# Optimization experiments

Hardware: AMD Instinct MI355X
Metric: run time of the kernel (lower is better)

The kernel has to match this reference:

```python
import jax, jax.numpy as jnp
import numpy as np
from jax import lax

B, H, W = 1, 128, 128
KS = 3
N = KS * KS  # 9 deformable sampling points
BN_EPS = 1e-5


def conv2d(x, w, padding=0, stride=1):
    return lax.conv_general_dilated(x, w, (stride, stride),
                                    [(padding, padding), (padding, padding)],
                                    dimension_numbers=('NCHW', 'OIHW', 'NCHW'))


def bn_eval(x, gamma, beta, mean, var):
    scale = gamma / jnp.sqrt(var + BN_EPS)
    return x * scale[None, :, None, None] + (beta - mean * scale)[None, :, None, None]


def upsample_bilinear_ac(x, oh, ow):
    # F.interpolate(mode='bilinear', align_corners=True), separable gather
    b, c, h, w = x.shape
    ys = jnp.linspace(0.0, h - 1.0, oh)
    xs = jnp.linspace(0.0, w - 1.0, ow)
    y0 = jnp.floor(ys).astype(jnp.int32)
    y1 = jnp.minimum(y0 + 1, h - 1)
    wy = (ys - y0).astype(x.dtype)[None, None, :, None]
    x0 = jnp.floor(xs).astype(jnp.int32)
    x1 = jnp.minimum(x0 + 1, w - 1)
    wx = (xs - x0).astype(x.dtype)
    r = x[:, :, y0, :] * (1.0 - wy) + x[:, :, y1, :] * wy
    return r[:, :, :, x0] * (1.0 - wx) + r[:, :, :, x1] * wx


def deform_conv(x, p_w, p_b, dc_w, pad=1):
    # DeformConv2d(inc, outc, ks=3, padding=1, modulation=False):
    # offsets from a 3x3 conv, bilinear gather at p0 + p_n + offset on the
    # zero-padded input, then 3x3 kernel contraction over the 9 samples.
    b, c, h, w = x.shape
    off = conv2d(x, p_w, padding=1) + p_b[None, :, None, None]  # (b, 2N, h, w)
    rng = jnp.arange(KS, dtype=x.dtype) - (KS - 1) // 2          # [-1, 0, 1]
    pnx, pny = jnp.meshgrid(rng, rng, indexing='ij')
    # absolute sampling coords in padded frame, (b, h, w, N)
    px = jnp.transpose(off[:, :N], (0, 2, 3, 1)) + pnx.ravel() + jnp.arange(1, h + 1, dtype=x.dtype)[None, :, None, None]
    py = jnp.transpose(off[:, N:], (0, 2, 3, 1)) + pny.ravel() + jnp.arange(1, w + 1, dtype=x.dtype)[None, None, :, None]
    Hp, Wp = h + 2 * pad, w + 2 * pad
    xp = jnp.pad(x, ((0, 0), (0, 0), (pad, pad), (pad, pad))).reshape(b, c, Hp * Wp)
    fx = jnp.floor(px)
    fy = jnp.floor(py)
    x0f = jnp.clip(fx, 0, Hp - 1)
    x1f = jnp.clip(fx + 1.0, 0, Hp - 1)
    y0f = jnp.clip(fy, 0, Wp - 1)
    y1f = jnp.clip(fy + 1.0, 0, Wp - 1)
    pxc = jnp.clip(px, 0, Hp - 1)
    pyc = jnp.clip(py, 0, Wp - 1)

    def gather(qxf, qyf):
        idx = (qxf.astype(jnp.int32) * Wp + qyf.astype(jnp.int32)).reshape(b, 1, h * w * N)
        g = jnp.take_along_axis(xp, jnp.broadcast_to(idx, (b, c, h * w * N)), axis=2)
        return g.reshape(b, c, h, w, N)

    g_lt = (1.0 + (x0f - pxc)) * (1.0 + (y0f - pyc))
    g_rb = (1.0 - (x1f - pxc)) * (1.0 - (y1f - pyc))
    g_lb = (1.0 + (x0f - pxc)) * (1.0 - (y1f - pyc))
    g_rt = (1.0 - (x1f - pxc)) * (1.0 + (y0f - pyc))
    x_off = (g_lt[:, None] * gather(x0f, y0f) + g_rb[:, None] * gather(x1f, y1f)
             + g_lb[:, None] * gather(x0f, y1f) + g_rt[:, None] * gather(x1f, y0f))
    # conv(kernel=3, stride=3) on the rearranged samples == contraction over N
    return jnp.einsum('bchwk,ock->bohw', x_off, dc_w.reshape(dc_w.shape[0], c, N))


def _forward(x, low_level_feat, fm_w, fs_w, p_w, p_b, dc_w,
             lc1_w, bn1_gamma, bn1_beta, bn1_mean, bn1_var,
             lc2_w, bn2_gamma, bn2_beta, bn2_mean, bn2_var):
    xu = upsample_bilinear_ac(x, H, W)                       # (B,256,128,128)
    Z = low_level_feat                                       # AdaptiveAvgPool2d((128,128)) is identity on 128x128 input
    v = jax.nn.sigmoid(jnp.einsum('oc,bchw->bohw', fm_w, Z))
    u = jnp.einsum('bchk,bckw->bchw', low_level_feat, v) + low_level_feat
    Cf = jnp.einsum('oc,bchw->bohw', fs_w, u)
    cc = jnp.concatenate([xu, Cf], axis=1)                   # (B,512,128,128)
    fam = deform_conv(cc, p_w, p_b, dc_w) + Cf
    up1 = jax.nn.relu(bn_eval(conv2d(fam, lc1_w, padding=1), bn1_gamma, bn1_beta, bn1_mean, bn1_var))
    up2 = jax.nn.relu(bn_eval(conv2d(up1, lc2_w, padding=1), bn2_gamma, bn2_beta, bn2_mean, bn2_var))
    return up1, up2


def setup_inputs():
    key = jax.random.key(0)
    ks = jax.random.split(key, 12)
    f32 = jnp.float32
    return {
        'x': jax.random.normal(ks[0], (B, 256, 32, 32), f32),
        'low_level_feat': jax.random.normal(ks[1], (B, 256, H, W), f32),
        'fm_w': jax.random.normal(ks[2], (256, 256), f32) * 0.0625,
        'fs_w': jax.random.normal(ks[3], (256, 256), f32) * 0.0625,
        'p_w': jax.random.normal(ks[4], (2 * N, 512, 3, 3), f32) * 0.01,
        'p_b': jnp.zeros((2 * N,), f32),
        'dc_w': jax.random.normal(ks[5], (256, 512, 3, 3), f32) * 0.02,
        'lc1_w': jax.random.normal(ks[6], (256, 256, 3, 3), f32) * 0.02,
        'bn1_gamma': jnp.ones((256,), f32),
        'bn1_beta': jnp.zeros((256,), f32),
        'bn1_mean': jax.random.normal(ks[7], (256,), f32) * 0.1,
        'bn1_var': jax.random.uniform(ks[8], (256,), f32) + 0.5,
        'lc2_w': jax.random.normal(ks[9], (256, 256, 3, 3), f32) * 0.02,
        'bn2_gamma': jnp.ones((256,), f32),
        'bn2_beta': jnp.zeros((256,), f32),
        'bn2_mean': jax.random.normal(ks[10], (256,), f32) * 0.1,
        'bn2_var': jax.random.uniform(ks[11], (256,), f32) + 0.5,
    }


def reference(x, low_level_feat, fm_w, fs_w, p_w, p_b, dc_w,
              lc1_w, bn1_gamma, bn1_beta, bn1_mean, bn1_var,
              lc2_w, bn2_gamma, bn2_beta, bn2_mean, bn2_var):
    return _forward(x, low_level_feat, fm_w, fs_w, p_w, p_b, dc_w,
                    lc1_w, bn1_gamma, bn1_beta, bn1_mean, bn1_var,
                    lc2_w, bn2_gamma, bn2_beta, bn2_mean, bn2_var)
```

## Files before the change

### kernel.cpp

```cpp
#include <hip/hip_runtime.h>
#include <math.h>

#define HW   16384
#define PS   16900

typedef __attribute__((ext_vector_type(8))) short bf16x8;
typedef __attribute__((ext_vector_type(4))) float f32x4;

__device__ inline unsigned short f2bf(float x) {
    unsigned int u = __float_as_uint(x);
    unsigned int r = (u + 0x7fffu + ((u >> 16) & 1u)) >> 16;
    return (unsigned short)r;
}
__device__ inline float bf2f(unsigned short h) {
    return __uint_as_float(((unsigned int)h) << 16);
}

__global__ __launch_bounds__(256) void zero_ringP2_k(unsigned short* __restrict__ b0,
                                                     unsigned short* __restrict__ b1) {
    int t = blockIdx.x * 256 + threadIdx.x;
    if (t >= 2 * 520 * 32) return;
    unsigned short* base = (t >= 520 * 32) ? b1 : b0;
    int tt = (t >= 520 * 32) ? t - 520 * 32 : t;
    int ck = (tt & 31) << 3, rp = tt >> 5;
    int row, col;
    if (rp < 130)      { row = 0;   col = rp; }
    else if (rp < 260) { row = 129; col = rp - 130; }
    else {
        int rem = rp - 260;
        if (rem >= 256) return;
        row = 1 + (rem >> 1); col = (rem & 1) ? 129 : 0;
    }
    bf16x8 z = (bf16x8){0, 0, 0, 0, 0, 0, 0, 0};
    *(bf16x8*)(base + (size_t)(row * 130 + col) * 256 + ck) = z;
}

__global__ __launch_bounds__(256) void ringT_k(unsigned short* __restrict__ ccT) {
    int t = blockIdx.x * 256 + threadIdx.x;
    if (t >= 520 * 256) return;
    int ci = t & 255, rp = t >> 8;
    int row, col;
    if (rp < 130)      { row = 0;   col = rp; }
    else if (rp < 260) { row = 129; col = rp - 130; }
    else {
        int rem = rp - 260;
        if (rem >= 256) return;
        row = 1 + (rem >> 1); col = (rem & 1) ? 129 : 0;
    }
    ccT[(size_t)(row * 130 + col) * 512 + 256 + ci] = 0;
}

__global__ __launch_bounds__(256) void xT_k(const float* __restrict__ x,
                                            float* __restrict__ xT) {
    int t = blockIdx.x * 256 + threadIdx.x;
    int c = t & 255, pos = t >> 8;
    xT[t] = x[(size_t)c * 1024 + pos];
}

__global__ __launch_bounds__(256) void up_cvtT_k(const float* __restrict__ xT,
                                                 unsigned short* __restrict__ ccT) {
    int pix = blockIdx.x;
    int c = threadIdx.x;
    int r = pix / 130, s = pix - r * 130;
    float val = 0.0f;
    if (r >= 1 && r <= 128 && s >= 1 && s <= 128) {
        int i = r - 1, j = s - 1;
        float yf = (float)i * (31.0f / 127.0f);
        float xf = (float)j * (31.0f / 127.0f);
        int y0 = min((int)yf, 31); int y1 = min(y0 + 1, 31);
        int x0 = min((int)xf, 31); int x1 = min(x0 + 1, 31);
        float wy = yf - (float)y0, wx = xf - (float)x0;
        float v00 = xT[(size_t)(y0 * 32 + x0) * 256 + c];
        float v01 = xT[(size_t)(y0 * 32 + x1) * 256 + c];
        float v10 = xT[(size_t)(y1 * 32 + x0) * 256 + c];
        float v11 = xT[(size_t)(y1 * 32 + x1) * 256 + c];
        float a = v00 * (1.0f - wx) + v01 * wx;
        float b = v10 * (1.0f - wx) + v11 * wx;
        val = a * (1.0f - wy) + b * wy;
    }
    ccT[(size_t)pix * 512 + c] = f2bf(val);
}

__global__ __launch_bounds__(256) void cvtT_tile_k(const float* __restrict__ src,
                                                   unsigned short* __restrict__ dst) {
    __shared__ float Ls[64][65];
    int px0 = blockIdx.x << 6;
    int c0  = blockIdx.y << 6;
    int t = threadIdx.x;
    int pxl = t & 63, cq = t >> 6;
#pragma unroll
    for (int it = 0; it < 16; ++it) {
        int cl = (it << 2) + cq;
        Ls[cl][pxl] = src[(size_t)(c0 + cl) * HW + px0 + pxl];
    }
    __syncthreads();
    int c8 = (t & 7) << 3;
    int pxb = t >> 3;
#pragma unroll
    for (int rr = 0; rr < 2; ++rr) {
        int px = pxb + (rr << 5);
        unsigned short pk[8];
#pragma unroll
        for (int e = 0; e < 8; ++e) pk[e] = f2bf(Ls[c8 + e][px]);
        *(bf16x8*)(dst + (size_t)(px0 + px) * 256 + c0 + c8) = *(bf16x8*)pk;
    }
}

__global__ __launch_bounds__(256) void w2bf_k(const float* __restrict__ a,
                                              const float* __restrict__ b,
                                              unsigned short* __restrict__ da,
                                              unsigned short* __restrict__ db) {
    int t = blockIdx.x * 256 + threadIdx.x;
    if (t >= 65536) return;
    da[t] = f2bf(a[t]);
    db[t] = f2bf(b[t]);
}

__global__ __launch_bounds__(256) void u_matmul_k(const float* __restrict__ llf,
                                                  const float* __restrict__ v,
                                                  float* __restrict__ u) {
    int c = blockIdx.y;
    const float* L = llf + (size_t)c * HW;
    const float* V = v   + (size_t)c * HW;
    float*       U = u   + (size_t)c * HW;
    int tid = threadIdx.x;
    int ty = tid >> 4, tx = tid & 15;
    int r0 = (blockIdx.x << 6) + (ty << 2);
    int w0 = tx << 3;
    float acc[4][8] = {};
    for (int k = 0; k < 128; ++k) {
        float a[4];
#pragma unroll
        for (int i = 0; i < 4; ++i) a[i] = L[(r0 + i) * 128 + k];
        float4 b0 = *(const float4*)(V + k * 128 + w0);
        float4 b1 = *(const float4*)(V + k * 128 + w0 + 4);
        float bv[8] = {b0.x, b0.y, b0.z, b0.w, b1.x, b1.y, b1.z, b1.w};
#pragma unroll
        for (int i = 0; i < 4; ++i)
#pragma unroll
            for (int j = 0; j < 8; ++j) acc[i][j] += a[i] * bv[j];
    }
#pragma unroll
    for (int i = 0; i < 4; ++i) {
#pragma unroll
        for (int j = 0; j < 8; ++j) acc[i][j] += L[(r0 + i) * 128 + w0 + j];
        *(float4*)(U + (r0 + i) * 128 + w0)     = make_float4(acc[i][0], acc[i][1], acc[i][2], acc[i][3]);
        *(float4*)(U + (r0 + i) * 128 + w0 + 4) = make_float4(acc[i][4], acc[i][5], acc[i][6], acc[i][7]);
    }
}

__global__ __launch_bounds__(256) void tr_dcwF9_k(const float* __restrict__ w,
                                                  unsigned short* __restrict__ dst) {
    int t = blockIdx.x * 256 + threadIdx.x;
    if (t >= 1179648) return;
    int e    = t & 7;
    int lane = (t >> 3) & 63;
    int f    = t >> 9;
    int mi   = f & 1;
    int s    = (f >> 1) & 1;
    int wv   = (f >> 2) & 7;
    int ch   = f >> 5;
    int kt   = ch >> 3;
    int o = (wv << 5) + (mi << 4) + (lane & 15);
    int c = ((ch & 7) << 6) + (s << 5) + ((lane >> 4) << 3) + e;
    dst[t] = f2bf(w[(size_t)o * 4608 + c * 9 + kt]);
}

__global__ __launch_bounds__(256) void tr_lcF2_k(const float* __restrict__ w1,
                                                 const float* __restrict__ w2,
                                                 unsigned short* __restrict__ d1,
                                                 unsigned short* __restrict__ d2) {
    const float* w = blockIdx.y ? w2 : w1;
    unsigned short* dst = blockIdx.y ? d2 : d1;
    int t = blockIdx.x * 256 + threadIdx.x;
    if (t >= 589824) return;
    int e    = t & 7;
    int lane = (t >> 3) & 63;
    int mi   = (t >> 9) & 3;
    int kss  = (t >> 11) & 7;
    int wo   = (t >> 14) & 3;
    int kt   = t >> 16;
    int o = (wo << 6) + (mi << 4) + (lane & 15);
    int c = (kss << 5) + ((lane >> 4) << 3) + e;
    dst[t] = f2bf(w[(size_t)o * 2304 + c * 9 + kt]);
}

__global__ __launch_bounds__(256) void tr_pw_k(const float* __restrict__ w,
                                               unsigned short* __restrict__ dst) {
    int t = blockIdx.x * 256 + threadIdx.x;
    if (t >= 9 * 32 * 512) return;
    int c = t & 511; int rest = t >> 9; int o = rest & 31; int k = rest >> 5;
    dst[t] = (o < 18) ? f2bf(w[(size_t)o * 4608 + c * 9 + k]) : (unsigned short)0;
}

__global__ __launch_bounds__(256, 2) void vmfma_k(
        const unsigned short* __restrict__ inT,
        const unsigned short* __restrict__ wh,
        float* __restrict__ vout) {
    __shared__ __align__(16) unsigned short Bs[32][72];
    int b = blockIdx.x;
    int xcd = b & 7, sl = b >> 3;
    int nt = (xcd << 6) + sl;
    int hrow = nt >> 2, pc0 = (nt & 3) << 5;
    int tid = threadIdx.x;
    int wv = tid >> 6, lane = tid & 63;
    int lr = lane & 15, lg = lane >> 4;
    int pxs = tid >> 3, cg8 = tid & 7;
    int p = (hrow << 7) + pc0 + pxs;
    f32x4 acc[4][2];
#pragma unroll
    for (int i = 0; i < 4; ++i)
#pragma unroll
        for (int j = 0; j < 2; ++j) acc[i][j] = (f32x4){0.f, 0.f, 0.f, 0.f};
    for (int ks = 0; ks < 256; ks += 64) {
        __syncthreads();
        *(bf16x8*)&Bs[pxs][cg8 << 3] =
            *(const bf16x8*)(inT + (size_t)p * 256 + ks + (cg8 << 3));
        __syncthreads();
#pragma unroll
        for (int s = 0; s < 2; ++s) {
            int ko = ks + (s << 5) + (lg << 3);
            bf16x8 af[4], bfr[2];
#pragma unroll
            for (int mi = 0; mi < 4; ++mi)
                af[mi] = *(const bf16x8*)(wh + (size_t)((wv << 6) + (mi << 4) + lr) * 256 + ko);
#pragma unroll
            for (int ni = 0; ni < 2; ++ni)
                bfr[ni] = *(const bf16x8*)(&Bs[(ni << 4) + lr][(s << 5) + (lg << 3)]);
#pragma unroll
            for (int mi = 0; mi < 4; ++mi)
#pragma unroll
                for (int ni = 0; ni < 2; ++ni)
                    acc[mi][ni] = __builtin_amdgcn_mfma_f32_16x16x32_bf16(
                        af[mi], bfr[ni], acc[mi][ni], 0, 0, 0);
        }
    }
#pragma unroll
    for (int mi = 0; mi < 4; ++mi)
#pragma unroll
        for (int ni = 0; ni < 2; ++ni)
#pragma unroll
            for (int r = 0; r < 4; ++r) {
                int o   = (wv << 6) + (mi << 4) + (lg << 2) + r;
                int pxx = pc0 + (ni << 4) + lr;
                vout[(size_t)o * HW + (hrow << 7) + pxx] =
                    1.0f / (1.0f + expf(-acc[mi][ni][r]));
            }
}

__global__ __launch_bounds__(256, 2) void cfmfma_k(
        const unsigned short* __restrict__ inT,
        const unsigned short* __restrict__ wh,
        unsigned short* __restrict__ ccT) {
    __shared__ __align__(16) unsigned short Bs[32][72];
    int b = blockIdx.x;
    int xcd = b & 7, sl = b >> 3;
    int nt = (xcd << 6) + sl;
    int hrow = nt >> 2, pc0 = (nt & 3) << 5;
    int tid = threadIdx.x;
    int wv = tid >> 6, lane = tid & 63;
    int lr = lane & 15, lg = lane >> 4;
    int pxs = tid >> 3, cg8 = tid & 7;
    int p = (hrow << 7) + pc0 + pxs;
    f32x4 acc[4][2];
#pragma unroll
    for (int i = 0; i < 4; ++i)
#pragma unroll
        for (int j = 0; j < 2; ++j) acc[i][j] = (f32x4){0.f, 0.f, 0.f, 0.f};
    for (int ks = 0; ks < 256; ks += 64) {
        __syncthreads();
        *(bf16x8*)&Bs[pxs][cg8 << 3] =
            *(const bf16x8*)(inT + (size_t)p * 256 + ks + (cg8 << 3));
        __syncthreads();
#pragma unroll
        for (int s = 0; s < 2; ++s) {
            int ko = ks + (s << 5) + (lg << 3);
            bf16x8 af[4], bfr[2];
#pragma unroll
            for (int mi = 0; mi < 4; ++mi)
                af[mi] = *(const bf16x8*)(wh + (size_t)((wv << 6) + (mi << 4) + lr) * 256 + ko);
#pragma unroll
            for (int ni = 0; ni < 2; ++ni)
                bfr[ni] = *(const bf16x8*)(&Bs[(ni << 4) + lr][(s << 5) + (lg << 3)]);
#pragma unroll
            for (int mi = 0; mi < 4; ++mi)
#pragma unroll
                for (int ni = 0; ni < 2; ++ni)
                    acc[mi][ni] = __builtin_amdgcn_mfma_f32_16x16x32_bf16(
                        af[mi], bfr[ni], acc[mi][ni], 0, 0, 0);
        }
    }
#pragma unroll
    for (int mi = 0; mi < 4; ++mi)
#pragma unroll
        for (int ni = 0; ni < 2; ++ni) {
            int pxx = pc0 + (ni << 4) + lr;
            int pix = (hrow + 1) * 130 + pxx + 1;
            unsigned short pk[4];
#pragma unroll
            for (int r = 0; r < 4; ++r) pk[r] = f2bf(acc[mi][ni][r]);
            *(ushort4*)(ccT + (size_t)pix * 512 + 256 + (wv << 6) + (mi << 4) + (lg << 2))
                = *(ushort4*)pk;
        }
}

__global__ __launch_bounds__(256, 2) void off_part2_k(
        const unsigned short* __restrict__ ccT,
        const unsigned short* __restrict__ pwTh,
        float* __restrict__ pbuf) {
    __shared__ __align__(16) unsigned short Ls[198][132];
    int b = blockIdx.x;
    int xcd = b & 7, slot = b >> 3;
    int hrow = (xcd << 4) + (slot >> 3);
    int rest = slot & 7;
    int pxh = rest >> 2, cg = rest & 3;
    int pc0h = pxh << 6, c0 = cg << 7;
    int tid = threadIdx.x;
    int wv = tid >> 6, lane = tid & 63;
    int lr = lane & 15, lg = lane >> 4;
    int wo = wv & 1;
    int pt0 = (wv >> 1) << 1;
    int chk = tid & 15, pxi0 = tid >> 4;
#pragma unroll
    for (int r = 0; r < 3; ++r) {
        const unsigned short* src = ccT + (size_t)((hrow + r) * 130 + pc0h) * 512 + c0;
        for (int pxi = pxi0; pxi < 66; pxi += 16)
            *(bf16x8*)&Ls[r * 66 + pxi][chk << 3] =
                *(const bf16x8*)(src + (size_t)pxi * 512 + (chk << 3));
    }
    __syncthreads();

    f32x4 acc[2];
    acc[0] = (f32x4){0.f, 0.f, 0.f, 0.f};
    acc[1] = (f32x4){0.f, 0.f, 0.f, 0.f};
    for (int kt = 0; kt < 9; ++kt) {
        int rowb = (kt / 3) * 66 + (kt % 3);
        const unsigned short* wk = pwTh + (size_t)kt * 16384
                                 + (size_t)((wo << 4) + lr) * 512 + c0;
#pragma unroll
        for (int ks = 0; ks < 128; ks += 32) {
            bf16x8 af = *(const bf16x8*)(wk + ks + (lg << 3));
#pragma unroll
            for (int pi = 0; pi < 2; ++pi) {
                int px = ((pt0 + pi) << 4) + lr;
                bf16x8 bfr = *(const bf16x8*)(&Ls[rowb + px][ks + (lg << 3)]);
                acc[pi] = __builtin_amdgcn_mfma_f32_16x16x32_bf16(af, bfr, acc[pi], 0, 0, 0);
            }
        }
    }
#pragma unroll
    for (int pi = 0; pi < 2; ++pi)
#pragma unroll
        for (int r = 0; r < 4; ++r) {
            int o = (wo << 4) + (lg << 2) + r;
            int p = (hrow << 7) + pc0h + ((pt0 + pi) << 4) + lr;
            pbuf[(size_t)((cg << 5) + o) * HW + p] = acc[pi][r];
        }
}

__global__ __launch_bounds__(256) void make_idx_k(const float* __restrict__ pbuf,
                                                  const float* __restrict__ pb,
                                                  int4* __restrict__ IDX,
                                                  float4* __restrict__ WT) {
    int t = blockIdx.x * 256 + threadIdx.x;
    if (t >= 9 * HW) return;
    int k = t >> 14, p = t & 16383;
    int h = p >> 7, w = p & 127;
    float ox = 0.f, oy = 0.f;
#pragma unroll
    for (int cg = 0; cg < 4; ++cg) {
        ox += pbuf[(size_t)((cg << 5) + k) * HW + p];
        oy += pbuf[(size_t)((cg << 5) + 9 + k) * HW + p];
    }
    float px = ox + pb[k]     + (float)(k / 3 - 1) + (float)(h + 1);
    float py = oy + pb[9 + k] + (float)(k % 3 - 1) + (float)(w + 1);
    float fx = floorf(px), fy = floorf(py);
    float x0 = fminf(fmaxf(fx,        0.f), 129.f);
    float x1 = fminf(fmaxf(fx + 1.0f, 0.f), 129.f);
    float y0 = fminf(fmaxf(fy,        0.f), 129.f);
    float y1 = fminf(fmaxf(fy + 1.0f, 0.f), 129.f);
    float pxc = fminf(fmaxf(px, 0.f), 129.f);
    float pyc = fminf(fmaxf(py, 0.f), 129.f);
    float gx0 = 1.0f + x0 - pxc, gx1 = 1.0f - x1 + pxc;
    float gy0 = 1.0f + y0 - pyc, gy1 = 1.0f - y1 + pyc;
    int ix0 = (int)x0, ix1 = (int)x1, iy0 = (int)y0, iy1 = (int)y1;
    IDX[t] = make_int4((ix0 * 130 + iy0) << 9, (ix1 * 130 + iy1) << 9,
                       (ix0 * 130 + iy1) << 9, (ix1 * 130 + iy0) << 9);
    WT[t]  = make_float4(gx0 * gy0, gx1 * gy1, gx0 * gy1, gx1 * gy0);
}

__global__ __launch_bounds__(512, 4) void fam9_k(
        const unsigned short* __restrict__ ccT,
        const unsigned short* __restrict__ dcwF,
        const int4* __restrict__ IDX, const float4* __restrict__ WT,
        unsigned short* __restrict__ part0,
        unsigned short* __restrict__ part1) {
    __shared__ __align__(16) unsigned short Bs[2][64][72];
    int b = blockIdx.x;
    int khalf = b >> 8;
    int bb = b & 255;
    int xcd = bb & 7, sl = bb >> 3;
    int nt = (xcd << 5) + sl;
    int hrow = nt >> 1, pc0 = (nt & 1) << 6;
    int tid = threadIdx.x;
    int wv = tid >> 6, lane = tid & 63;
    int lr = lane & 15, lg = lane >> 4;
    int pxg = tid >> 3, grp = tid & 7;
    int p2 = (hrow << 7) + pc0 + pxg;
    const unsigned short* wfb = dcwF + ((size_t)wv << 11) + ((size_t)lane << 3);
    f32x4 acc[2][4];
#pragma unroll
    for (int i = 0; i < 2; ++i)
#pragma unroll
        for (int j = 0; j < 4; ++j) acc[i][j] = (f32x4){0.f, 0.f, 0.f, 0.f};

    bf16x8 v0, v1, v2, v3;
    bf16x8 Aa00, Aa01, Aa10, Aa11;
    bf16x8 Ba00, Ba01, Ba10, Ba11;

#define ISSUE_A9(S, ch) do {                                                  \
    const unsigned short* ap_ = wfb + ((size_t)(ch) << 14);                   \
    S##00 = *(const bf16x8*)(ap_);                                            \
    S##01 = *(const bf16x8*)(ap_ + 512);                                      \
    S##10 = *(const bf16x8*)(ap_ + 1024);                                     \
    S##11 = *(const bf16x8*)(ap_ + 1536);                                     \
} while (0)

#define ISSUE_G9(ch, idm) do {                                                \
    int cb_ = (((ch) & 7) << 6) + (grp << 3);                                 \
    v0 = *(const bf16x8*)(ccT + (idm).x + cb_);                               \
    v1 = *(const bf16x8*)(ccT + (idm).y + cb_);                               \
    v2 = *(const bf16x8*)(ccT + (idm).z + cb_);                               \
    v3 = *(const bf16x8*)(ccT + (idm).w + cb_);                               \
} while (0)

#define NEXT_G9(cn) do {                                                      \
    if ((cn) < c1) {                                                          \
        if (((cn) & 7) == 0) {                                                \
            idc = idn; wtc = wtn;                                             \
            int kt2_ = ((cn) >> 3) + 1;                                       \
            if ((kt2_ << 3) < c1) {                                           \
                idn = IDX[(kt2_ << 14) + p2];                                 \
                wtn = WT [(kt2_ << 14) + p2];                                 \
            }                                                                 \
        }                                                                     \
        ISSUE_G9(cn, idc);                                                    \
        wnext = wtc;                                                          \
    }                                                                         \
} while (0)

#define PUBLISH9(bi) do {                                                     \
    unsigned short pk_[8];                                                    \
    _Pragma("unroll")                                                         \
    for (int e_ = 0; e_ < 8; ++e_) {                                          \
        float val_ = wcur.x * bf2f((unsigned short)v0[e_])                    \
                   + wcur.y * bf2f((unsigned short)v1[e_])                    \
                   + wcur.z * bf2f((unsigned short)v2[e_])                    \
                   + wcur.w * bf2f((unsigned short)v3[e_]);                   \
        pk_[e_] = f2bf(val_);                                                 \
    }                                                                         \
    *(bf16x8*)&Bs[bi][pxg][grp << 3] = *(bf16x8*)pk_;                         \
} while (0)

#define MFMA9(S, bi) do {                                                     \
    _Pragma("unroll")                                                         \
    for (int ni_ = 0; ni_ < 4; ++ni_) {                                       \
        bf16x8 b0_ = *(const bf16x8*)(&Bs[bi][(ni_ << 4) + lr][lg << 3]);     \
        acc[0][ni_] = __builtin_amdgcn_mfma_f32_16x16x32_bf16(S##00, b0_, acc[0][ni_], 0, 0, 0); \
        acc[1][ni_] = __builtin_amdgcn_mfma_f32_16x16x32_bf16(S##01, b0_, acc[1][ni_], 0, 0, 0); \
    }                                                                         \
    _Pragma("unroll")                                                         \
    for (int ni_ = 0; ni_ < 4; ++ni_) {                                       \
        bf16x8 b1_ = *(const bf16x8*)(&Bs[bi][(ni_ << 4) + lr][32 + (lg << 3)]); \
        acc[0][ni_] = __builtin_amdgcn_mfma_f32_16x16x32_bf16(S##10, b1_, acc[0][ni_], 0, 0, 0); \
        acc[1][ni_] = __builtin_amdgcn_mfma_f32_16x16x32_bf16(S##11, b1_, acc[1][ni_], 0, 0, 0); \
    }                                                                         \
} while (0)

    int c0 = khalf * 36, c1 = c0 + 36;
    int kt0 = c0 >> 3;
    int4   idc = IDX[(kt0 << 14) + p2];
    float4 wtc = WT [(kt0 << 14) + p2];
    int4   idn = IDX[((kt0 + 1) << 14) + p2];
    float4 wtn = WT [((kt0 + 1) << 14) + p2];
    ISSUE_G9(c0, idc);
    float4 wcur = wtc, wnext = wtc;
    ISSUE_A9(Aa, c0);

    for (int c = c0; c < c1; c += 2) {
        PUBLISH9(0);
        NEXT_G9(c + 1);
        ISSUE_A9(Ba, c + 1);
        __syncthreads();
        MFMA9(Aa, 0);
        wcur = wnext;
        PUBLISH9(1);
        NEXT_G9(c + 2);
        if (c + 2 < c1) ISSUE_A9(Aa, c + 2);
        __syncthreads();
        MFMA9(Ba, 1);
        wcur = wnext;
    }
#undef ISSUE_A9
#undef ISSUE_G9
#undef NEXT_G9
#undef PUBLISH9
#undef MFMA9

    unsigned short* pt = khalf ? part1 : part0;
#pragma unroll
    for (int mi = 0; mi < 2; ++mi)
#pragma unroll
        for (int ni = 0; ni < 4; ++ni) {
            int pxx = pc0 + (ni << 4) + lr;
            int p = (hrow << 7) + pxx;
            unsigned short pk[4];
#pragma unroll
            for (int r = 0; r < 4; ++r) pk[r] = f2bf(acc[mi][ni][r]);
            *(ushort4*)(pt + (size_t)p * 256 + (wv << 5) + (mi << 4) + (lg << 2))
                = *(ushort4*)pk;
        }
}

__global__ __launch_bounds__(256) void combineT_k(
        const unsigned short* __restrict__ p0,
        const unsigned short* __restrict__ p1,
        const unsigned short* __restrict__ ccT,
        unsigned short* __restrict__ famT) {
    int t = blockIdx.x * 256 + threadIdx.x;
    int o8 = (t & 31) << 3, p = t >> 5;
    int row = p >> 7, col = p & 127;
    int pix = (row + 1) * 130 + col + 1;
    bf16x8 a = *(const bf16x8*)(p0 + (size_t)p * 256 + o8);
    bf16x8 b = *(const bf16x8*)(p1 + (size_t)p * 256 + o8);
    bf16x8 c = *(const bf16x8*)(ccT + (size_t)pix * 512 + 256 + o8);
    unsigned short out[8];
#pragma unroll
    for (int e = 0; e < 8; ++e)
        out[e] = f2bf(bf2f((unsigned short)a[e]) + bf2f((unsigned short)b[e])
                      + bf2f((unsigned short)c[e]));
    *(bf16x8*)(famT + (size_t)pix * 256 + o8) = *(bf16x8*)out;
}

__global__ __launch_bounds__(256, 2) void conv2T_k(
        const unsigned short* __restrict__ inT,
        const unsigned short* __restrict__ wF,
        const float* __restrict__ gam, const float* __restrict__ bet,
        const float* __restrict__ mean, const float* __restrict__ var,
        float* __restrict__ out_flat,
        unsigned short* __restrict__ out_padT) {
    __shared__ __align__(16) unsigned short Ls[102][264];
    __shared__ float scs[256], bis[256];
    int b = blockIdx.x;
    int xcd = b & 7, slot = b >> 3;
    int nt = (xcd << 6) + slot;
    int hrow = nt >> 2, pc0 = (nt & 3) << 5;
    int tid = threadIdx.x;
    int wv = tid >> 6, lane = tid & 63;
    int lr = lane & 15, lg = lane >> 4;
    {
        float sc = gam[tid] * rsqrtf(var[tid] + 1e-5f);
        scs[tid] = sc;
        bis[tid] = bet[tid] - mean[tid] * sc;
    }
#pragma unroll
    for (int r = 0; r < 3; ++r) {
        const unsigned short* src = inT + (size_t)((hrow + r) * 130 + pc0) * 256;
#pragma unroll
        for (int ps = 0; ps < 5; ++ps) {
            int idx = ps * 2048 + tid * 8;
            if (idx < 8704) {
                bf16x8 v = *(const bf16x8*)(src + idx);
                *(bf16x8*)&Ls[r * 34 + (idx >> 8)][idx & 255] = v;
            }
        }
    }
    __syncthreads();

    f32x4 acc[4][2];
#pragma unroll
    for (int i = 0; i < 4; ++i)
#pragma unroll
        for (int j = 0; j < 2; ++j) acc[i][j] = (f32x4){0.f, 0.f, 0.f, 0.f};

    const unsigned short* wvb = wF + ((size_t)wv << 14) + ((size_t)lane << 3);
    for (int kt = 0; kt < 9; ++kt) {
        int rowb = (kt / 3) * 34 + (kt % 3);
        const unsigned short* wkb = wvb + (size_t)kt * 65536;
#pragma unroll
        for (int kss = 0; kss < 8; ++kss) {
            int ks = kss << 5;
            bf16x8 af[4], bfr[2];
#pragma unroll
            for (int mi = 0; mi < 4; ++mi)
                af[mi] = *(const bf16x8*)(wkb + (size_t)kss * 2048 + mi * 512);
#pragma unroll
            for (int ni = 0; ni < 2; ++ni)
                bfr[ni] = *(const bf16x8*)(&Ls[rowb + (ni << 4) + lr][ks + (lg << 3)]);
#pragma unroll
            for (int mi = 0; mi < 4; ++mi)
#pragma unroll
                for (int ni = 0; ni < 2; ++ni)
                    acc[mi][ni] = __builtin_amdgcn_mfma_f32_16x16x32_bf16(
                        af[mi], bfr[ni], acc[mi][ni], 0, 0, 0);
        }
    }

#pragma unroll
    for (int mi = 0; mi < 4; ++mi)
#pragma unroll
        for (int ni = 0; ni < 2; ++ni) {
            int pxx = pc0 + (ni << 4) + lr;
            unsigned short pk[4];
#pragma unroll
            for (int r = 0; r < 4; ++r) {
                int o = (wv << 6) + (mi << 4) + (lg << 2) + r;
                float rv = fmaxf(acc[mi][ni][r] * scs[o] + bis[o], 0.0f);
                out_flat[(size_t)o * HW + (hrow << 7) + pxx] = rv;
                pk[r] = f2bf(rv);
            }
            if (out_padT) {
                int pix = (hrow + 1) * 130 + pxx + 1;
                *(ushort4*)(out_padT + (size_t)pix * 256 + (wv << 6) + (mi << 4) + (lg << 2))
                    = *(ushort4*)pk;
            }
        }
}

extern "C" void kernel_launch(void* const* d_in, const int* in_sizes, int n_in,
                              void* d_out, int out_size, void* d_ws, size_t ws_size,
                              hipStream_t stream) {
    const float* x     = (const float*)d_in[0];
    const float* llf   = (const float*)d_in[1];
    const float* fm_w  = (const float*)d_in[2];
    const float* fs_w  = (const float*)d_in[3];
    const float* p_w   = (const float*)d_in[4];
    const float* p_b   = (const float*)d_in[5];
    const float* dc_w  = (const float*)d_in[6];
    const float* lc1_w = (const float*)d_in[7];
    const float* bn1g  = (const float*)d_in[8];
    const float* bn1b  = (const float*)d_in[9];
    const float* bn1m  = (const float*)d_in[10];
    const float* bn1v  = (const float*)d_in[11];
    const float* lc2_w = (const float*)d_in[12];
    const float* bn2g  = (const float*)d_in[13];
    const float* bn2b  = (const float*)d_in[14];
    const float* bn2m  = (const float*)d_in[15];
    const float* bn2v  = (const float*)d_in[16];
    float* out1 = (float*)d_out;
    float* out2 = out1 + (size_t)256 * HW;

    if (ws_size < 79839232u) return;
    char* ws = (char*)d_ws;
    unsigned short* ccT   = (unsigned short*)ws;
    float*          xTf   = (float*)(ws + 17305600);
    float*          vbuf  = (float*)(ws + 17305600);
    unsigned short* famT  = (unsigned short*)(ws + 17305600);
    unsigned short* up1T  = (unsigned short*)(ws + 26091520);
    unsigned short* llfT  = (unsigned short*)(ws + 34877440);
    unsigned short* uT    = (unsigned short*)(ws + 43266048);
    unsigned short* part0 = (unsigned short*)(ws + 43266048);
    unsigned short* fmwh  = (unsigned short*)(ws + 51654656);
    unsigned short* fswh  = (unsigned short*)(ws + 51785728);
    float*          ubuf  = (float*)(ws + 51916800);
    float*          pbuf  = (float*)(ws + 51916800);
    unsigned short* part1 = (unsigned short*)(ws + 51916800);
    int4*           IDX   = (int4*)  (ws + 60305408);
    float4*         WT    = (float4*)(ws + 62664704);
    unsigned short* dcwF   = (unsigned short*)(ws + 68694016);
    unsigned short* lcw1F  = (unsigned short*)(ws + 71053312);
    unsigned short* lcw2F  = (unsigned short*)(ws + 72232960);
    unsigned short* pwTh   = (unsigned short*)(ws + 73412608);

    xT_k<<<dim3(1024), 256, 0, stream>>>(x, xTf);
    up_cvtT_k<<<dim3(16900), 256, 0, stream>>>(xTf, ccT);
    cvtT_tile_k<<<dim3(256, 4), 256, 0, stream>>>(llf, llfT);
    w2bf_k<<<dim3(256), 256, 0, stream>>>(fm_w, fs_w, fmwh, fswh);
    vmfma_k<<<dim3(512), 256, 0, stream>>>(llfT, fmwh, vbuf);
    u_matmul_k<<<dim3(2, 256), 256, 0, stream>>>(llf, vbuf, ubuf);
    cvtT_tile_k<<<dim3(256, 4), 256, 0, stream>>>(ubuf, uT);
    tr_dcwF9_k<<<dim3(4608), 256, 0, stream>>>(dc_w, dcwF);
    tr_lcF2_k<<<dim3(2304, 2), 256, 0, stream>>>(lc1_w, lc2_w, lcw1F, lcw2F);
    tr_pw_k<<<dim3(576), 256, 0, stream>>>(p_w, pwTh);
    cfmfma_k<<<dim3(512), 256, 0, stream>>>(uT, fswh, ccT);
    ringT_k<<<dim3(520), 256, 0, stream>>>(ccT);
    off_part2_k<<<dim3(1024), 256, 0, stream>>>(ccT, pwTh, pbuf);
    make_idx_k<<<dim3(576), 256, 0, stream>>>(pbuf, p_b, IDX, WT);
    zero_ringP2_k<<<dim3(130), 256, 0, stream>>>(famT, up1T);
    fam9_k<<<dim3(512), 512, 0, stream>>>(ccT, dcwF, IDX, WT, part0, part1);
    combineT_k<<<dim3(2048), 256, 0, stream>>>(part0, part1, ccT, famT);
    conv2T_k<<<dim3(512), 256, 0, stream>>>(famT, lcw1F, bn1g, bn1b, bn1m, bn1v,
                                            out1, up1T);
    conv2T_k<<<dim3(512), 256, 0, stream>>>(up1T, lcw2F, bn2g, bn2b, bn2m, bn2v,
                                            out2, nullptr);
}
```

Baseline: 396.8 us.

## Fuse partial-sum combine into first conv, stage full K in LDS for 1x1 MFMAs

Removes the separate combineT kernel and famT buffer by summing part0, part1 and the ccT residual while loading the first 3x3 conv tile into LDS, with zero padding handled inline. The 1x1 MFMA kernels now load the whole 256-channel pixel tile into shared memory once, replacing four sync-separated chunk loads. The u_matmul inner loop reads L with float4 loads. This saves a launch and a round trip through global memory for the combined feature map, but the first conv's prologue now reads three sources per element and the larger LDS tile may lower occupancy.

```diff
diff --git a/kernel.cpp b/kernel.cpp
--- a/kernel.cpp
+++ b/kernel.cpp
@@ -16,13 +16,10 @@
     return __uint_as_float(((unsigned int)h) << 16);
 }
 
-__global__ __launch_bounds__(256) void zero_ringP2_k(unsigned short* __restrict__ b0,
-                                                     unsigned short* __restrict__ b1) {
+__global__ __launch_bounds__(256) void zero_ringP_k(unsigned short* __restrict__ base) {
     int t = blockIdx.x * 256 + threadIdx.x;
-    if (t >= 2 * 520 * 32) return;
-    unsigned short* base = (t >= 520 * 32) ? b1 : b0;
-    int tt = (t >= 520 * 32) ? t - 520 * 32 : t;
-    int ck = (tt & 31) << 3, rp = tt >> 5;
+    if (t >= 520 * 32) return;
+    int ck = (t & 31) << 3, rp = t >> 5;
     int row, col;
     if (rp < 130)      { row = 0;   col = rp; }
     else if (rp < 260) { row = 129; col = rp - 130; }
@@ -128,17 +125,21 @@
     int r0 = (blockIdx.x << 6) + (ty << 2);
     int w0 = tx << 3;
     float acc[4][8] = {};
-    for (int k = 0; k < 128; ++k) {
-        float a[4];
-#pragma unroll
-        for (int i = 0; i < 4; ++i) a[i] = L[(r0 + i) * 128 + k];
-        float4 b0 = *(const float4*)(V + k * 128 + w0);
-        float4 b1 = *(const float4*)(V + k * 128 + w0 + 4);
-        float bv[8] = {b0.x, b0.y, b0.z, b0.w, b1.x, b1.y, b1.z, b1.w};
-#pragma unroll
-        for (int i = 0; i < 4; ++i)
-#pragma unroll
-            for (int j = 0; j < 8; ++j) acc[i][j] += a[i] * bv[j];
+    for (int k4 = 0; k4 < 128; k4 += 4) {
+        float4 a4[4];
+#pragma unroll
+        for (int i = 0; i < 4; ++i) a4[i] = *(const float4*)(L + (r0 + i) * 128 + k4);
+#pragma unroll
+        for (int e = 0; e < 4; ++e) {
+            float4 b0 = *(const float4*)(V + (k4 + e) * 128 + w0);
+            float4 b1 = *(const float4*)(V + (k4 + e) * 128 + w0 + 4);
+            float bv[8] = {b0.x, b0.y, b0.z, b0.w, b1.x, b1.y, b1.z, b1.w};
+            float ae[4] = {a4[0][e], a4[1][e], a4[2][e], a4[3][e]};
+#pragma unroll
+            for (int i = 0; i < 4; ++i)
+#pragma unroll
+                for (int j = 0; j < 8; ++j) acc[i][j] += ae[i] * bv[j];
+        }
     }
 #pragma unroll
     for (int i = 0; i < 4; ++i) {
@@ -193,11 +194,11 @@
     dst[t] = (o < 18) ? f2bf(w[(size_t)o * 4608 + c * 9 + k]) : (unsigned short)0;
 }
 
-__global__ __launch_bounds__(256, 2) void vmfma_k(
+__global__ __launch_bounds__(256, 2) void vmfma2_k(
         const unsigned short* __restrict__ inT,
         const unsigned short* __restrict__ wh,
         float* __restrict__ vout) {
-    __shared__ __align__(16) unsigned short Bs[32][72];
+    __shared__ __align__(16) unsigned short Bs[32][264];
     int b = blockIdx.x;
     int xcd = b & 7, sl = b >> 3;
     int nt = (xcd << 6) + sl;
@@ -205,35 +206,35 @@
     int tid = threadIdx.x;
     int wv = tid >> 6, lane = tid & 63;
     int lr = lane & 15, lg = lane >> 4;
-    int pxs = tid >> 3, cg8 = tid & 7;
-    int p = (hrow << 7) + pc0 + pxs;
+    int pbase = (hrow << 7) + pc0;
+#pragma unroll
+    for (int ps = 0; ps < 4; ++ps) {
+        int idx = ps * 2048 + tid * 8;
+        int px = idx >> 8, ch = idx & 255;
+        *(bf16x8*)&Bs[px][ch] = *(const bf16x8*)(inT + (size_t)(pbase + px) * 256 + ch);
+    }
+    __syncthreads();
     f32x4 acc[4][2];
 #pragma unroll
     for (int i = 0; i < 4; ++i)
 #pragma unroll
         for (int j = 0; j < 2; ++j) acc[i][j] = (f32x4){0.f, 0.f, 0.f, 0.f};
-    for (int ks = 0; ks < 256; ks += 64) {
-        __syncthreads();
-        *(bf16x8*)&Bs[pxs][cg8 << 3] =
-            *(const bf16x8*)(inT + (size_t)p * 256 + ks + (cg8 << 3));
-        __syncthreads();
-#pragma unroll
-        for (int s = 0; s < 2; ++s) {
-            int ko = ks + (s << 5) + (lg << 3);
-            bf16x8 af[4], bfr[2];
-#pragma unroll
-            for (int mi = 0; mi < 4; ++mi)
-                af[mi] = *(const bf16x8*)(wh + (size_t)((wv << 6) + (mi << 4) + lr) * 256 + ko);
+#pragma unroll
+    for (int kss = 0; kss < 8; ++kss) {
+        int ks = kss << 5;
+        bf16x8 af[4], bfr[2];
+#pragma unroll
+        for (int mi = 0; mi < 4; ++mi)
+            af[mi] = *(const bf16x8*)(wh + (size_t)((wv << 6) + (mi << 4) + lr) * 256 + ks + (lg << 3));
+#pragma unroll
+        for (int ni = 0; ni < 2; ++ni)
+            bfr[ni] = *(const bf16x8*)(&Bs[(ni << 4) + lr][ks + (lg << 3)]);
+#pragma unroll
+        for (int mi = 0; mi < 4; ++mi)
 #pragma unroll
             for (int ni = 0; ni < 2; ++ni)
-                bfr[ni] = *(const bf16x8*)(&Bs[(ni << 4) + lr][(s << 5) + (lg << 3)]);
-#pragma unroll
-            for (int mi = 0; mi < 4; ++mi)
-#pragma unroll
-                for (int ni = 0; ni < 2; ++ni)
-                    acc[mi][ni] = __builtin_amdgcn_mfma_f32_16x16x32_bf16(
-                        af[mi], bfr[ni], acc[mi][ni], 0, 0, 0);
-        }
+                acc[mi][ni] = __builtin_amdgcn_mfma_f32_16x16x32_bf16(
+                    af[mi], bfr[ni], acc[mi][ni], 0, 0, 0);
     }
 #pragma unroll
     for (int mi = 0; mi < 4; ++mi)
@@ -248,11 +249,11 @@
             }
 }
 
-__global__ __launch_bounds__(256, 2) void cfmfma_k(
+__global__ __launch_bounds__(256, 2) void cfmfma2_k(
         const unsigned short* __restrict__ inT,
         const unsigned short* __restrict__ wh,
         unsigned short* __restrict__ ccT) {
-    __shared__ __align__(16) unsigned short Bs[32][72];
+    __shared__ __align__(16) unsigned short Bs[32][264];
     int b = blockIdx.x;
     int xcd = b & 7, sl = b >> 3;
     int nt = (xcd << 6) + sl;
@@ -260,35 +261,35 @@
     int tid = threadIdx.x;
     int wv = tid >> 6, lane = tid & 63;
     int lr = lane & 15, lg = lane >> 4;
-    int pxs = tid >> 3, cg8 = tid & 7;
-    int p = (hrow << 7) + pc0 + pxs;
+    int pbase = (hrow << 7) + pc0;
+#pragma unroll
+    for (int ps = 0; ps < 4; ++ps) {
+        int idx = ps * 2048 + tid * 8;
+        int px = idx >> 8, ch = idx & 255;
+        *(bf16x8*)&Bs[px][ch] = *(const bf16x8*)(inT + (size_t)(pbase + px) * 256 + ch);
+    }
+    __syncthreads();
     f32x4 acc[4][2];
 #pragma unroll
     for (int i = 0; i < 4; ++i)
 #pragma unroll
         for (int j = 0; j < 2; ++j) acc[i][j] = (f32x4){0.f, 0.f, 0.f, 0.f};
-    for (int ks = 0; ks < 256; ks += 64) {
-        __syncthreads();
-        *(bf16x8*)&Bs[pxs][cg8 << 3] =
-            *(const bf16x8*)(inT + (size_t)p * 256 + ks + (cg8 << 3));
-        __syncthreads();
-#pragma unroll
-        for (int s = 0; s < 2; ++s) {
-            int ko = ks + (s << 5) + (lg << 3);
-            bf16x8 af[4], bfr[2];
-#pragma unroll
-            for (int mi = 0; mi < 4; ++mi)
-                af[mi] = *(const bf16x8*)(wh + (size_t)((wv << 6) + (mi << 4) + lr) * 256 + ko);
+#pragma unroll
+    for (int kss = 0; kss < 8; ++kss) {
+        int ks = kss << 5;
+        bf16x8 af[4], bfr[2];
+#pragma unroll
+        for (int mi = 0; mi < 4; ++mi)
+            af[mi] = *(const bf16x8*)(wh + (size_t)((wv << 6) + (mi << 4) + lr) * 256 + ks + (lg << 3));
+#pragma unroll
+        for (int ni = 0; ni < 2; ++ni)
+            bfr[ni] = *(const bf16x8*)(&Bs[(ni << 4) + lr][ks + (lg << 3)]);
+#pragma unroll
+        for (int mi = 0; mi < 4; ++mi)
 #pragma unroll
             for (int ni = 0; ni < 2; ++ni)
-                bfr[ni] = *(const bf16x8*)(&Bs[(ni << 4) + lr][(s << 5) + (lg << 3)]);
-#pragma unroll
-            for (int mi = 0; mi < 4; ++mi)
-#pragma unroll
-                for (int ni = 0; ni < 2; ++ni)
-                    acc[mi][ni] = __builtin_amdgcn_mfma_f32_16x16x32_bf16(
-                        af[mi], bfr[ni], acc[mi][ni], 0, 0, 0);
-        }
+                acc[mi][ni] = __builtin_amdgcn_mfma_f32_16x16x32_bf16(
+                    af[mi], bfr[ni], acc[mi][ni], 0, 0, 0);
     }
 #pragma unroll
     for (int mi = 0; mi < 4; ++mi)
@@ -522,28 +523,10 @@
         }
 }
 
-__global__ __launch_bounds__(256) void combineT_k(
+__global__ __launch_bounds__(256, 2) void conv2c_k(
         const unsigned short* __restrict__ p0,
         const unsigned short* __restrict__ p1,
         const unsigned short* __restrict__ ccT,
-        unsigned short* __restrict__ famT) {
-    int t = blockIdx.x * 256 + threadIdx.x;
-    int o8 = (t & 31) << 3, p = t >> 5;
-    int row = p >> 7, col = p & 127;
-    int pix = (row + 1) * 130 + col + 1;
-    bf16x8 a = *(const bf16x8*)(p0 + (size_t)p * 256 + o8);
-    bf16x8 b = *(const bf16x8*)(p1 + (size_t)p * 256 + o8);
-    bf16x8 c = *(const bf16x8*)(ccT + (size_t)pix * 512 + 256 + o8);
-    unsigned short out[8];
-#pragma unroll
-    for (int e = 0; e < 8; ++e)
-        out[e] = f2bf(bf2f((unsigned short)a[e]) + bf2f((unsigned short)b[e])
-                      + bf2f((unsigned short)c[e]));
-    *(bf16x8*)(famT + (size_t)pix * 256 + o8) = *(bf16x8*)out;
-}
-
-__global__ __launch_bounds__(256, 2) void conv2T_k(
-        const unsigned short* __restrict__ inT,
         const unsigned short* __restrict__ wF,
         const float* __restrict__ gam, const float* __restrict__ bet,
         const float* __restrict__ mean, const float* __restrict__ var,
@@ -565,6 +548,102 @@
     }
 #pragma unroll
     for (int r = 0; r < 3; ++r) {
+        int rr = hrow + r;
+#pragma unroll
+        for (int ps = 0; ps < 5; ++ps) {
+            int idx = ps * 2048 + tid * 8;
+            if (idx < 8704) {
+                int pxi = idx >> 8, ch = idx & 255;
+                int cc = pc0 + pxi;
+                bf16x8 v = (bf16x8){0, 0, 0, 0, 0, 0, 0, 0};
+                if (rr >= 1 && rr <= 128 && cc >= 1 && cc <= 128) {
+                    int p = ((rr - 1) << 7) + (cc - 1);
+                    bf16x8 a  = *(const bf16x8*)(p0 + (size_t)p * 256 + ch);
+                    bf16x8 bb = *(const bf16x8*)(p1 + (size_t)p * 256 + ch);
+                    bf16x8 cf = *(const bf16x8*)(ccT + (size_t)(rr * 130 + cc) * 512 + 256 + ch);
+                    unsigned short pk[8];
+#pragma unroll
+                    for (int e = 0; e < 8; ++e)
+                        pk[e] = f2bf(bf2f((unsigned short)a[e]) + bf2f((unsigned short)bb[e])
+                                     + bf2f((unsigned short)cf[e]));
+                    v = *(bf16x8*)pk;
+                }
+                *(bf16x8*)&Ls[r * 34 + pxi][ch] = v;
+            }
+        }
+    }
+    __syncthreads();
+
+    f32x4 acc[4][2];
+#pragma unroll
+    for (int i = 0; i < 4; ++i)
+#pragma unroll
+        for (int j = 0; j < 2; ++j) acc[i][j] = (f32x4){0.f, 0.f, 0.f, 0.f};
+
+    const unsigned short* wvb = wF + ((size_t)wv << 14) + ((size_t)lane << 3);
+    for (int kt = 0; kt < 9; ++kt) {
+        int rowb = (kt / 3) * 34 + (kt % 3);
+        const unsigned short* wkb = wvb + (size_t)kt * 65536;
+#pragma unroll
+        for (int kss = 0; kss < 8; ++kss) {
+            int ks = kss << 5;
+            bf16x8 af[4], bfr[2];
+#pragma unroll
+            for (int mi = 0; mi < 4; ++mi)
+                af[mi] = *(const bf16x8*)(wkb + (size_t)kss * 2048 + mi * 512);
+#pragma unroll
+            for (int ni = 0; ni < 2; ++ni)
+                bfr[ni] = *(const bf16x8*)(&Ls[rowb + (ni << 4) + lr][ks + (lg << 3)]);
+#pragma unroll
+            for (int mi = 0; mi < 4; ++mi)
+#pragma unroll
+                for (int ni = 0; ni < 2; ++ni)
+                    acc[mi][ni] = __builtin_amdgcn_mfma_f32_16x16x32_bf16(
+                        af[mi], bfr[ni], acc[mi][ni], 0, 0, 0);
+        }
+    }
+
+#pragma unroll
+    for (int mi = 0; mi < 4; ++mi)
+#pragma unroll
+        for (int ni = 0; ni < 2; ++ni) {
+            int pxx = pc0 + (ni << 4) + lr;
+            unsigned short pk[4];
+#pragma unroll
+            for (int r = 0; r < 4; ++r) {
+                int o = (wv << 6) + (mi << 4) + (lg << 2) + r;
+                float rv = fmaxf(acc[mi][ni][r] * scs[o] + bis[o], 0.0f);
+                out_flat[(size_t)o * HW + (hrow << 7) + pxx] = rv;
+                pk[r] = f2bf(rv);
+            }
+            int pix = (hrow + 1) * 130 + pxx + 1;
+            *(ushort4*)(out_padT + (size_t)pix * 256 + (wv << 6) + (mi << 4) + (lg << 2))
+                = *(ushort4*)pk;
+        }
+}
+
+__global__ __launch_bounds__(256, 2) void conv2T_k(
+        const unsigned short* __restrict__ inT,
+        const unsigned short* __restrict__ wF,
+        const float* __restrict__ gam, const float* __restrict__ bet,
+        const float* __restrict__ mean, const float* __restrict__ var,
+        float* __restrict__ out_flat) {
+    __shared__ __align__(16) unsigned short Ls[102][264];
+    __shared__ float scs[256], bis[256];
+    int b = blockIdx.x;
+    int xcd = b & 7, slot = b >> 3;
+    int nt = (xcd << 6) + slot;
+    int hrow = nt >> 2, pc0 = (nt & 3) << 5;
+    int tid = threadIdx.x;
+    int wv = tid >> 6, lane = tid & 63;
+    int lr = lane & 15, lg = lane >> 4;
+    {
+        float sc = gam[tid] * rsqrtf(var[tid] + 1e-5f);
+        scs[tid] = sc;
+        bis[tid] = bet[tid] - mean[tid] * sc;
+    }
+#pragma unroll
+    for (int r = 0; r < 3; ++r) {
         const unsigned short* src = inT + (size_t)((hrow + r) * 130 + pc0) * 256;
 #pragma unroll
         for (int ps = 0; ps < 5; ++ps) {
@@ -611,18 +690,11 @@
 #pragma unroll
         for (int ni = 0; ni < 2; ++ni) {
             int pxx = pc0 + (ni << 4) + lr;
-            unsigned short pk[4];
 #pragma unroll
             for (int r = 0; r < 4; ++r) {
                 int o = (wv << 6) + (mi << 4) + (lg << 2) + r;
                 float rv = fmaxf(acc[mi][ni][r] * scs[o] + bis[o], 0.0f);
                 out_flat[(size_t)o * HW + (hrow << 7) + pxx] = rv;
-                pk[r] = f2bf(rv);
-            }
-            if (out_padT) {
-                int pix = (hrow + 1) * 130 + pxx + 1;
-                *(ushort4*)(out_padT + (size_t)pix * 256 + (wv << 6) + (mi << 4) + (lg << 2))
-                    = *(ushort4*)pk;
             }
         }
 }
@@ -655,7 +727,6 @@
     unsigned short* ccT   = (unsigned short*)ws;
     float*          xTf   = (float*)(ws + 17305600);
     float*          vbuf  = (float*)(ws + 17305600);
-    unsigned short* famT  = (unsigned short*)(ws + 17305600);
     unsigned short* up1T  = (unsigned short*)(ws + 26091520);
     unsigned short* llfT  = (unsigned short*)(ws + 34877440);
     unsigned short* uT    = (unsigned short*)(ws + 43266048);
@@ -676,21 +747,20 @@
     up_cvtT_k<<<dim3(16900), 256, 0, stream>>>(xTf, ccT);
     cvtT_tile_k<<<dim3(256, 4), 256, 0, stream>>>(llf, llfT);
     w2bf_k<<<dim3(256), 256, 0, stream>>>(fm_w, fs_w, fmwh, fswh);
-    vmfma_k<<<dim3(512), 256, 0, stream>>>(llfT, fmwh, vbuf);
+    vmfma2_k<<<dim3(512), 256, 0, stream>>>(llfT, fmwh, vbuf);
     u_matmul_k<<<dim3(2, 256), 256, 0, stream>>>(llf, vbuf, ubuf);
     cvtT_tile_k<<<dim3(256, 4), 256, 0, stream>>>(ubuf, uT);
     tr_dcwF9_k<<<dim3(4608), 256, 0, stream>>>(dc_w, dcwF);
     tr_lcF2_k<<<dim3(2304, 2), 256, 0, stream>>>(lc1_w, lc2_w, lcw1F, lcw2F);
     tr_pw_k<<<dim3(576), 256, 0, stream>>>(p_w, pwTh);
-    cfmfma_k<<<dim3(512), 256, 0, stream>>>(uT, fswh, ccT);
+    cfmfma2_k<<<dim3(512), 256, 0, stream>>>(uT, fswh, ccT);
     ringT_k<<<dim3(520), 256, 0, stream>>>(ccT);
     off_part2_k<<<dim3(1024), 256, 0, stream>>>(ccT, pwTh, pbuf);
     make_idx_k<<<dim3(576), 256, 0, stream>>>(pbuf, p_b, IDX, WT);
-    zero_ringP2_k<<<dim3(130), 256, 0, stream>>>(famT, up1T);
+    zero_ringP_k<<<dim3(65), 256, 0, stream>>>(up1T);
     fam9_k<<<dim3(512), 512, 0, stream>>>(ccT, dcwF, IDX, WT, part0, part1);
-    combineT_k<<<dim3(2048), 256, 0, stream>>>(part0, part1, ccT, famT);
-    conv2T_k<<<dim3(512), 256, 0, stream>>>(famT, lcw1F, bn1g, bn1b, bn1m, bn1v,
-                                            out1, up1T);
+    conv2c_k<<<dim3(512), 256, 0, stream>>>(part0, part1, ccT, lcw1F,
+                                            bn1g, bn1b, bn1m, bn1v, out1, up1T);
     conv2T_k<<<dim3(512), 256, 0, stream>>>(up1T, lcw2F, bn2g, bn2b, bn2m, bn2v,
-                                            out2, nullptr);
-}
+                                            out2);
+}
```

Result: slower. 410.3 us (+3.4%).
